# Performance work log

Measured on AMD Instinct MI355X. Metric: run time of the kernel, lower is better.

The kernel has to match this reference:

```python
import jax, jax.numpy as jnp
import numpy as np

WINDOW = 11
SIGMA = 1.5
K1 = 0.01
K2 = 0.03
L = 1.0


def _gauss_kernel(dtype):
    coords = jnp.arange(WINDOW, dtype=dtype) - (WINDOW - 1) / 2.0
    g = jnp.exp(-coords ** 2 / (2.0 * SIGMA ** 2))
    g = g / g.sum()
    return jnp.outer(g, g)  # [k, k]


def setup_inputs() -> dict:
    key = jax.random.key(0)
    k1, k2 = jax.random.split(key)
    B, T, H, W = 8, 16, 256, 256
    return {
        "predicted": jax.random.normal(k1, (B, T, H, W, 1), dtype=jnp.float32),
        "target": jax.random.normal(k2, (B, T, H, W, 1), dtype=jnp.float32),
    }


def reference(predicted, target):
    B, T, H, W, C = predicted.shape
    dt = predicted.dtype
    eps = jnp.asarray(1e-6, dt)

    # valid mask: samples whose target sums to zero are excluded (weighted mean)
    valid = (jnp.sum(target, axis=(1, 2, 3, 4)) != 0).astype(dt)  # [B]

    # per-sample, per-channel min-max normalization over (T, H, W)
    def norm(x):
        mn = jnp.min(x, axis=(1, 2, 3), keepdims=True)
        mx = jnp.max(x, axis=(1, 2, 3), keepdims=True)
        return (x - mn) / jnp.maximum(mx - mn, eps)

    p = norm(predicted)
    t = norm(target)

    # batch all (B,T) single-channel images through one conv: NCHW with N = B*T
    img1 = t.reshape(B * T, 1, H, W)  # original uses target as img1
    img2 = p.reshape(B * T, 1, H, W)
    kern = _gauss_kernel(dt).reshape(1, 1, WINDOW, WINDOW)
    pad = WINDOW // 2

    def conv(x):
        return jax.lax.conv_general_dilated(x, kern, (1, 1), [(pad, pad), (pad, pad)])

    mu1 = conv(img1)
    mu2 = conv(img2)
    mu1_sq = mu1 * mu1
    mu2_sq = mu2 * mu2
    mu1_mu2 = mu1 * mu2
    sigma1_sq = jnp.maximum(conv(img1 * img1) - mu1_sq, eps)
    sigma2_sq = jnp.maximum(conv(img2 * img2) - mu2_sq, eps)
    sigma12 = conv(img1 * img2) - mu1_mu2

    C1 = (K1 * L) ** 2
    C2 = (K2 * L) ** 2
    C3 = C2 / 2.0
    root = jnp.sqrt(sigma1_sq * sigma2_sq)
    luminance = (2.0 * mu1_mu2 + C1) / (mu1_sq + mu2_sq + C1)
    contrast = (2.0 * root + C2) / (sigma1_sq + sigma2_sq + C2)
    structure = (sigma12 + C3) / (root + C3)
    ssim_map = luminance * contrast * structure  # [B*T, 1, H, W]

    # per-(b,t) pixel mean, then mean over T == mean over (T,H,W)
    ssim_per_sample = ssim_map.reshape(B, T, H, W).mean(axis=(1, 2, 3))  # [B]

    n_valid = jnp.maximum(jnp.sum(valid), jnp.asarray(1.0, dt))
    loss = jnp.sum((1.0 - ssim_per_sample) * valid) / n_valid
    return loss
```

## Files before the change

kernel.cpp:

```cpp
#include <hip/hip_runtime.h>
#include <math.h>

#define BB 8
#define TT 16
#define HH 256
#define WW 256
#define NPX (TT * HH * WW)
#define CROWS 32
#define NBLK (BB * TT * (HH / CROWS))

#define P_MINP 0
#define P_MAXP 512
#define P_MINT 1024
#define P_MAXT 1536
#define P_SUMT 2048
#define WS_S   2560

typedef float v2f __attribute__((ext_vector_type(2)));

#define G0 0.0010283776f
#define G1 0.0075987582f
#define G2 0.0360008014f
#define G3 0.1093606427f
#define G4 0.2130055745f
#define G5 0.2660117857f
#define GA_(k) ((k) == 0 || (k) == 10 ? G0 : (k) == 1 || (k) == 9 ? G1 \
              : (k) == 2 || (k) == 8 ? G2 : (k) == 3 || (k) == 7 ? G3 \
              : (k) == 4 || (k) == 6 ? G4 : G5)

__global__ __launch_bounds__(256) void k_reduce(const float* __restrict__ p,
                                                const float* __restrict__ t,
                                                float* __restrict__ wsf) {
  const int b = blockIdx.x >> 6;
  const size_t base = (size_t)b * NPX + (size_t)(blockIdx.x & 63) * (NPX / 64);
  const int tid = threadIdx.x;

  float mnp = 3.4e38f, mxp = -3.4e38f, mnt = 3.4e38f, mxt = -3.4e38f, st = 0.f;
  const float4* p4 = (const float4*)(p + base);
  const float4* t4 = (const float4*)(t + base);
#pragma unroll 4
  for (int it = 0; it < 16; ++it) {
    float4 a = p4[it * 256 + tid];
    float4 c = t4[it * 256 + tid];
    mnp = fminf(mnp, fminf(fminf(a.x, a.y), fminf(a.z, a.w)));
    mxp = fmaxf(mxp, fmaxf(fmaxf(a.x, a.y), fmaxf(a.z, a.w)));
    mnt = fminf(mnt, fminf(fminf(c.x, c.y), fminf(c.z, c.w)));
    mxt = fmaxf(mxt, fmaxf(fmaxf(c.x, c.y), fmaxf(c.z, c.w)));
    st += c.x + c.y + c.z + c.w;
  }
  for (int off = 32; off > 0; off >>= 1) {
    mnp = fminf(mnp, __shfl_down(mnp, off));
    mxp = fmaxf(mxp, __shfl_down(mxp, off));
    mnt = fminf(mnt, __shfl_down(mnt, off));
    mxt = fmaxf(mxt, __shfl_down(mxt, off));
    st += __shfl_down(st, off);
  }
  __shared__ float s_mnp[4], s_mxp[4], s_mnt[4], s_mxt[4], s_st[4];
  int wave = tid >> 6, lane = tid & 63;
  if (lane == 0) {
    s_mnp[wave] = mnp; s_mxp[wave] = mxp;
    s_mnt[wave] = mnt; s_mxt[wave] = mxt; s_st[wave] = st;
  }
  __syncthreads();
  if (tid == 0) {
    for (int w = 1; w < 4; ++w) {
      mnp = fminf(mnp, s_mnp[w]); mxp = fmaxf(mxp, s_mxp[w]);
      mnt = fminf(mnt, s_mnt[w]); mxt = fmaxf(mxt, s_mxt[w]);
      st += s_st[w];
    }
    wsf[P_MINP + blockIdx.x] = mnp;
    wsf[P_MAXP + blockIdx.x] = mxp;
    wsf[P_MINT + blockIdx.x] = mnt;
    wsf[P_MAXT + blockIdx.x] = mxt;
    wsf[P_SUMT + blockIdx.x] = st;
    if (blockIdx.x == 0) wsf[WS_S] = 0.f;
  }
}

#define STEP(J) do {                                                         \
    constexpr int jj = (J);                                                  \
    constexpr int buf = jj & 1;                                              \
    constexpr int slot = jj % 11;                                            \
    const bool in = (unsigned)(ystart + jj) < (unsigned)HH;                  \
    v2f nv;                                                                  \
    nv.x = in ? fmaf(tcur, ts, tb) : 0.f;                                    \
    nv.y = in ? fmaf(pcur, ps, pb) : 0.f;                                    \
    srow[buf][x + 5] = nv;                                                   \
    if constexpr (jj < 41) {                                                 \
      const int yn = min(max(ystart + jj + 1, 0), HH - 1);                   \
      tnxt = tptr[(size_t)yn * WW + x];                                      \
      pnxt = pptr[(size_t)yn * WW + x];                                      \
    }                                                                        \
    __syncthreads();                                                         \
    v2f hmu = {0.f, 0.f}, hsq = {0.f, 0.f};                                  \
    float htp = 0.f;                                                         \
    _Pragma("unroll")                                                        \
    for (int k = 0; k < 11; ++k) {                                           \
      v2f v = srow[buf][x + k];                                              \
      v2f g2 = {GA_(k), GA_(k)};                                             \
      v2f w = g2 * v;                                                        \
      hmu = hmu + w;                                                         \
      hsq = __builtin_elementwise_fma(w, v, hsq);                            \
      htp = fmaf(w.x, v.y, htp);                                             \
    }                                                                        \
    r_mu[slot] = hmu; r_sq[slot] = hsq; r_tp[slot] = htp;                    \
    if constexpr (jj >= 10) {                                                \
      v2f vmu = {0.f, 0.f}, vsq = {0.f, 0.f};                                \
      float vtp = 0.f;                                                       \
      _Pragma("unroll")                                                      \
      for (int k = 0; k < 11; ++k) {                                         \
        const int s = (jj + 1 + k) % 11;                                     \
        v2f g2 = {GA_(k), GA_(k)};                                           \
        vmu = __builtin_elementwise_fma(g2, r_mu[s], vmu);                   \
        vsq = __builtin_elementwise_fma(g2, r_sq[s], vsq);                   \
        vtp = fmaf(GA_(k), r_tp[s], vtp);                                    \
      }                                                                      \
      float m1 = vmu.x, m2 = vmu.y;                                          \
      float mu11 = m1 * m1, mu22 = m2 * m2, m12 = m1 * m2;                   \
      float s1 = fmaxf(vsq.x - mu11, 1e-6f);                                 \
      float s2 = fmaxf(vsq.y - mu22, 1e-6f);                                 \
      float s12 = vtp - m12;                                                 \
      float root = sqrtf(s1 * s2);                                           \
      float num = fmaf(2.f, m12, C1) * fmaf(2.f, root, C2) * (s12 + C3);     \
      float den = (mu11 + mu22 + C1) * (s1 + s2 + C2) * (root + C3);         \
      acc = fmaf(num, __builtin_amdgcn_rcpf(den), acc);                      \
    }                                                                        \
    tcur = tnxt; pcur = pnxt;                                                \
    __builtin_amdgcn_sched_barrier(0);                                       \
  } while (0)

__global__ __launch_bounds__(256, 3) void k_ssim(const float* __restrict__ pred,
                                                 const float* __restrict__ targ,
                                                 float* __restrict__ wsf) {
  const int img = blockIdx.x >> 3;
  const int chunk = blockIdx.x & 7;
  const int b = img >> 4;
  const int x = threadIdx.x;
  const int y0 = chunk * CROWS;
  const float* tptr = targ + (size_t)img * (HH * WW);
  const float* pptr = pred + (size_t)img * (HH * WW);

  __shared__ float sprm[5];
  if (x < 64) {
    float mnp = wsf[P_MINP + b * 64 + x];
    float mxp = wsf[P_MAXP + b * 64 + x];
    float mnt = wsf[P_MINT + b * 64 + x];
    float mxt = wsf[P_MAXT + b * 64 + x];
    float st  = wsf[P_SUMT + b * 64 + x];
    for (int off = 32; off > 0; off >>= 1) {
      mnp = fminf(mnp, __shfl_down(mnp, off));
      mxp = fmaxf(mxp, __shfl_down(mxp, off));
      mnt = fminf(mnt, __shfl_down(mnt, off));
      mxt = fmaxf(mxt, __shfl_down(mxt, off));
      st += __shfl_down(st, off);
    }
    if (x == 0) {
      float psv = 1.f / fmaxf(mxp - mnp, 1e-6f);
      float tsv = 1.f / fmaxf(mxt - mnt, 1e-6f);
      sprm[0] = psv; sprm[1] = -mnp * psv;
      sprm[2] = tsv; sprm[3] = -mnt * tsv;
      sprm[4] = (st != 0.f) ? 1.f : 0.f;
    }
  }

  __shared__ v2f srow[2][WW + 12];
  if (x < 5) {
    v2f z = {0.f, 0.f};
    srow[0][x] = z; srow[1][x] = z;
    srow[0][WW + 5 + x] = z; srow[1][WW + 5 + x] = z;
  }
  __syncthreads();
  const float ps = sprm[0], pb = sprm[1], ts = sprm[2], tb = sprm[3];

  v2f r_mu[11], r_sq[11];
  float r_tp[11];
  float acc = 0.f;
  const int ystart = y0 - 5;
  const float C1 = 1e-4f, C2 = 9e-4f, C3 = 4.5e-4f;

  float tcur, pcur, tnxt = 0.f, pnxt = 0.f;
  {
    const int yc = min(max(ystart, 0), HH - 1);
    tcur = tptr[(size_t)yc * WW + x];
    pcur = pptr[(size_t)yc * WW + x];
  }

  STEP(0);  STEP(1);  STEP(2);  STEP(3);  STEP(4);  STEP(5);  STEP(6);
  STEP(7);  STEP(8);  STEP(9);  STEP(10); STEP(11); STEP(12); STEP(13);
  STEP(14); STEP(15); STEP(16); STEP(17); STEP(18); STEP(19); STEP(20);
  STEP(21); STEP(22); STEP(23); STEP(24); STEP(25); STEP(26); STEP(27);
  STEP(28); STEP(29); STEP(30); STEP(31); STEP(32); STEP(33); STEP(34);
  STEP(35); STEP(36); STEP(37); STEP(38); STEP(39); STEP(40); STEP(41);

  for (int off = 32; off > 0; off >>= 1) acc += __shfl_down(acc, off);
  __shared__ float sred[4];
  if ((x & 63) == 0) sred[x >> 6] = acc;
  __syncthreads();
  if (x == 0) {
    float v = sred[0] + sred[1] + sred[2] + sred[3];
    atomicAdd(&wsf[WS_S], v * sprm[4]);
  }
}

__global__ void k_loss(const float* __restrict__ wsf, float* __restrict__ out) {
  const int c = threadIdx.x;
  float sums[8];
#pragma unroll
  for (int b = 0; b < 8; ++b) sums[b] = wsf[P_SUMT + b * 64 + c];
  for (int off = 32; off > 0; off >>= 1) {
#pragma unroll
    for (int b = 0; b < 8; ++b) sums[b] += __shfl_down(sums[b], off);
  }
  if (c == 0) {
    float sv = 0.f;
#pragma unroll
    for (int b = 0; b < 8; ++b) sv += (sums[b] != 0.f) ? 1.f : 0.f;
    float S = wsf[WS_S];
    out[0] = (sv - S * (1.f / (float)NPX)) / fmaxf(sv, 1.f);
  }
}

extern "C" void kernel_launch(void* const* d_in, const int* in_sizes, int n_in,
                              void* d_out, int out_size, void* d_ws, size_t ws_size,
                              hipStream_t stream) {
  const float* pred = (const float*)d_in[0];
  const float* targ = (const float*)d_in[1];
  float* wsf = (float*)d_ws;
  float* out = (float*)d_out;

  hipLaunchKernelGGL(k_reduce, dim3(512), dim3(256), 0, stream, pred, targ, wsf);
  hipLaunchKernelGGL(k_ssim, dim3(NBLK), dim3(256), 0, stream, pred, targ, wsf);
  hipLaunchKernelGGL(k_loss, dim3(1), dim3(64), 0, stream, wsf, out);
}
```

Before: 132.5 us.

## Halve SSIM row chunk, raise occupancy, fold loss kernel into last block

Cuts rows per block from 32 to 16, doubling the grid and raising the launch-bounds occupancy target from 3 to 6 blocks per CU. The final loss computation moves into the last-finishing SSIM block through an atomic counter, which removes one kernel launch. The sched_barrier mask is loosened so the compiler can move some instructions across steps. In exchange, the 10-row halo is now recomputed over 26 steps for 16 output rows instead of 42 steps for 32, so redundant vertical work rises sharply, and register pressure is capped tighter.

```diff
diff --git a/kernel.cpp b/kernel.cpp
--- a/kernel.cpp
+++ b/kernel.cpp
@@ -6,7 +6,8 @@
 #define HH 256
 #define WW 256
 #define NPX (TT * HH * WW)
-#define CROWS 32
+#define CROWS 16
+#define NSTEP (CROWS + 10)
 #define NBLK (BB * TT * (HH / CROWS))
 
 #define P_MINP 0
@@ -15,6 +16,7 @@
 #define P_MAXT 1536
 #define P_SUMT 2048
 #define WS_S   2560
+#define WS_CNT 2561
 
 typedef float v2f __attribute__((ext_vector_type(2)));
 
@@ -73,7 +75,10 @@
     wsf[P_MINT + blockIdx.x] = mnt;
     wsf[P_MAXT + blockIdx.x] = mxt;
     wsf[P_SUMT + blockIdx.x] = st;
-    if (blockIdx.x == 0) wsf[WS_S] = 0.f;
+    if (blockIdx.x == 0) {
+      wsf[WS_S] = 0.f;
+      ((unsigned*)wsf)[WS_CNT] = 0u;
+    }
   }
 }
 
@@ -86,7 +91,7 @@
     nv.x = in ? fmaf(tcur, ts, tb) : 0.f;                                    \
     nv.y = in ? fmaf(pcur, ps, pb) : 0.f;                                    \
     srow[buf][x + 5] = nv;                                                   \
-    if constexpr (jj < 41) {                                                 \
+    if constexpr (jj < NSTEP - 1) {                                          \
       const int yn = min(max(ystart + jj + 1, 0), HH - 1);                   \
       tnxt = tptr[(size_t)yn * WW + x];                                      \
       pnxt = pptr[(size_t)yn * WW + x];                                      \
@@ -126,14 +131,15 @@
       acc = fmaf(num, __builtin_amdgcn_rcpf(den), acc);                      \
     }                                                                        \
     tcur = tnxt; pcur = pnxt;                                                \
-    __builtin_amdgcn_sched_barrier(0);                                       \
+    __builtin_amdgcn_sched_barrier(0x0007);                                  \
   } while (0)
 
-__global__ __launch_bounds__(256, 3) void k_ssim(const float* __restrict__ pred,
+__global__ __launch_bounds__(256, 6) void k_ssim(const float* __restrict__ pred,
                                                  const float* __restrict__ targ,
-                                                 float* __restrict__ wsf) {
-  const int img = blockIdx.x >> 3;
-  const int chunk = blockIdx.x & 7;
+                                                 float* __restrict__ wsf,
+                                                 float* __restrict__ out) {
+  const int img = blockIdx.x >> 4;
+  const int chunk = blockIdx.x & 15;
   const int b = img >> 4;
   const int x = threadIdx.x;
   const int y0 = chunk * CROWS;
@@ -188,35 +194,39 @@
   STEP(0);  STEP(1);  STEP(2);  STEP(3);  STEP(4);  STEP(5);  STEP(6);
   STEP(7);  STEP(8);  STEP(9);  STEP(10); STEP(11); STEP(12); STEP(13);
   STEP(14); STEP(15); STEP(16); STEP(17); STEP(18); STEP(19); STEP(20);
-  STEP(21); STEP(22); STEP(23); STEP(24); STEP(25); STEP(26); STEP(27);
-  STEP(28); STEP(29); STEP(30); STEP(31); STEP(32); STEP(33); STEP(34);
-  STEP(35); STEP(36); STEP(37); STEP(38); STEP(39); STEP(40); STEP(41);
+  STEP(21); STEP(22); STEP(23); STEP(24); STEP(25);
 
   for (int off = 32; off > 0; off >>= 1) acc += __shfl_down(acc, off);
   __shared__ float sred[4];
+  __shared__ bool sdone;
   if ((x & 63) == 0) sred[x >> 6] = acc;
   __syncthreads();
   if (x == 0) {
     float v = sred[0] + sred[1] + sred[2] + sred[3];
     atomicAdd(&wsf[WS_S], v * sprm[4]);
-  }
-}
-
-__global__ void k_loss(const float* __restrict__ wsf, float* __restrict__ out) {
-  const int c = threadIdx.x;
-  float sums[8];
+    __threadfence();
+    unsigned n = atomicAdd(&((unsigned*)wsf)[WS_CNT], 1u);
+    sdone = (n == NBLK - 1);
+  }
+  __syncthreads();
+  if (sdone) {
+    __threadfence();
+    float sums[8];
+    if (x < 64) {
 #pragma unroll
-  for (int b = 0; b < 8; ++b) sums[b] = wsf[P_SUMT + b * 64 + c];
-  for (int off = 32; off > 0; off >>= 1) {
+      for (int sb = 0; sb < 8; ++sb) sums[sb] = wsf[P_SUMT + sb * 64 + x];
+      for (int off = 32; off > 0; off >>= 1) {
 #pragma unroll
-    for (int b = 0; b < 8; ++b) sums[b] += __shfl_down(sums[b], off);
-  }
-  if (c == 0) {
-    float sv = 0.f;
+        for (int sb = 0; sb < 8; ++sb) sums[sb] += __shfl_down(sums[sb], off);
+      }
+    }
+    if (x == 0) {
+      float sv = 0.f;
 #pragma unroll
-    for (int b = 0; b < 8; ++b) sv += (sums[b] != 0.f) ? 1.f : 0.f;
-    float S = wsf[WS_S];
-    out[0] = (sv - S * (1.f / (float)NPX)) / fmaxf(sv, 1.f);
+      for (int sb = 0; sb < 8; ++sb) sv += (sums[sb] != 0.f) ? 1.f : 0.f;
+      float S = atomicAdd(&wsf[WS_S], 0.f);
+      out[0] = (sv - S * (1.f / (float)NPX)) / fmaxf(sv, 1.f);
+    }
   }
 }
 
@@ -229,6 +239,5 @@
   float* out = (float*)d_out;
 
   hipLaunchKernelGGL(k_reduce, dim3(512), dim3(256), 0, stream, pred, targ, wsf);
-  hipLaunchKernelGGL(k_ssim, dim3(NBLK), dim3(256), 0, stream, pred, targ, wsf);
-  hipLaunchKernelGGL(k_loss, dim3(1), dim3(64), 0, stream, wsf, out);
+  hipLaunchKernelGGL(k_ssim, dim3(NBLK), dim3(256), 0, stream, pred, targ, wsf, out);
 }
```

After: 237.6 us. 79.4% more time.

## Batch four rows per barrier with 8-slot LDS ring and deeper prefetch

Applied to the files above, without the earlier changes.

Restructures the per-row loop so each phase prefetches four input rows into registers, computes four rows from shared memory, then writes the next four normalized rows and syncs once. This cuts block barriers from one per row to one per four rows, and raises the global-load prefetch distance to hide latency. In exchange it needs an 8-slot shared-memory ring instead of double buffering, plus extra prefetch registers, which may reduce occupancy under the 3-blocks launch bound.

```diff
diff --git a/kernel.cpp b/kernel.cpp
--- a/kernel.cpp
+++ b/kernel.cpp
@@ -7,6 +7,8 @@
 #define WW 256
 #define NPX (TT * HH * WW)
 #define CROWS 32
+#define NROWS (CROWS + 10)
+#define NSLOT 8
 #define NBLK (BB * TT * (HH / CROWS))
 
 #define P_MINP 0
@@ -77,56 +79,64 @@
   }
 }
 
-#define STEP(J) do {                                                         \
-    constexpr int jj = (J);                                                  \
-    constexpr int buf = jj & 1;                                              \
-    constexpr int slot = jj % 11;                                            \
-    const bool in = (unsigned)(ystart + jj) < (unsigned)HH;                  \
-    v2f nv;                                                                  \
-    nv.x = in ? fmaf(tcur, ts, tb) : 0.f;                                    \
-    nv.y = in ? fmaf(pcur, ps, pb) : 0.f;                                    \
-    srow[buf][x + 5] = nv;                                                   \
-    if constexpr (jj < 41) {                                                 \
-      const int yn = min(max(ystart + jj + 1, 0), HH - 1);                   \
-      tnxt = tptr[(size_t)yn * WW + x];                                      \
-      pnxt = pptr[(size_t)yn * WW + x];                                      \
-    }                                                                        \
-    __syncthreads();                                                         \
-    v2f hmu = {0.f, 0.f}, hsq = {0.f, 0.f};                                  \
-    float htp = 0.f;                                                         \
-    _Pragma("unroll")                                                        \
-    for (int k = 0; k < 11; ++k) {                                           \
-      v2f v = srow[buf][x + k];                                              \
-      v2f g2 = {GA_(k), GA_(k)};                                             \
-      v2f w = g2 * v;                                                        \
-      hmu = hmu + w;                                                         \
-      hsq = __builtin_elementwise_fma(w, v, hsq);                            \
-      htp = fmaf(w.x, v.y, htp);                                             \
-    }                                                                        \
-    r_mu[slot] = hmu; r_sq[slot] = hsq; r_tp[slot] = htp;                    \
-    if constexpr (jj >= 10) {                                                \
-      v2f vmu = {0.f, 0.f}, vsq = {0.f, 0.f};                                \
-      float vtp = 0.f;                                                       \
-      _Pragma("unroll")                                                      \
-      for (int k = 0; k < 11; ++k) {                                         \
-        const int s = (jj + 1 + k) % 11;                                     \
-        v2f g2 = {GA_(k), GA_(k)};                                           \
-        vmu = __builtin_elementwise_fma(g2, r_mu[s], vmu);                   \
-        vsq = __builtin_elementwise_fma(g2, r_sq[s], vsq);                   \
-        vtp = fmaf(GA_(k), r_tp[s], vtp);                                    \
-      }                                                                      \
-      float m1 = vmu.x, m2 = vmu.y;                                          \
-      float mu11 = m1 * m1, mu22 = m2 * m2, m12 = m1 * m2;                   \
-      float s1 = fmaxf(vsq.x - mu11, 1e-6f);                                 \
-      float s2 = fmaxf(vsq.y - mu22, 1e-6f);                                 \
-      float s12 = vtp - m12;                                                 \
-      float root = sqrtf(s1 * s2);                                           \
-      float num = fmaf(2.f, m12, C1) * fmaf(2.f, root, C2) * (s12 + C3);     \
-      float den = (mu11 + mu22 + C1) * (s1 + s2 + C2) * (root + C3);         \
-      acc = fmaf(num, __builtin_amdgcn_rcpf(den), acc);                      \
-    }                                                                        \
-    tcur = tnxt; pcur = pnxt;                                                \
-    __builtin_amdgcn_sched_barrier(0);                                       \
+
+#define LOADR(R) do { constexpr int r_ = (R); if constexpr (r_ < NROWS) {     \
+    const int yc_ = min(max(ystart + r_, 0), HH - 1);                          \
+    tpre[r_ & 3] = tptr[(size_t)yc_ * WW + x];                                 \
+    ppre[r_ & 3] = pptr[(size_t)yc_ * WW + x];                                 \
+  } } while (0)
+
+#define WRITER(R) do { constexpr int r_ = (R); if constexpr (r_ < NROWS) {     \
+    const bool in_ = (unsigned)(ystart + r_) < (unsigned)HH;                   \
+    v2f nv_;                                                                   \
+    nv_.x = in_ ? fmaf(tpre[r_ & 3], ts, tb) : 0.f;                            \
+    nv_.y = in_ ? fmaf(ppre[r_ & 3], ps, pb) : 0.f;                            \
+    srow[r_ & (NSLOT - 1)][x + 5] = nv_;                                       \
+  } } while (0)
+
+#define CSTEP(R) do { constexpr int r_ = (R); if constexpr (r_ < NROWS) {      \
+    constexpr int slot_ = r_ % 11;                                             \
+    v2f hmu = {0.f, 0.f}, hsq = {0.f, 0.f};                                    \
+    float htp = 0.f;                                                           \
+    _Pragma("unroll")                                                          \
+    for (int k = 0; k < 11; ++k) {                                             \
+      v2f v = srow[r_ & (NSLOT - 1)][x + k];                                   \
+      v2f g2 = {GA_(k), GA_(k)};                                               \
+      v2f w = g2 * v;                                                          \
+      hmu = hmu + w;                                                           \
+      hsq = __builtin_elementwise_fma(w, v, hsq);                              \
+      htp = fmaf(w.x, v.y, htp);                                               \
+    }                                                                          \
+    r_mu[slot_] = hmu; r_sq[slot_] = hsq; r_tp[slot_] = htp;                   \
+    if constexpr (r_ >= 10) {                                                  \
+      v2f vmu = {0.f, 0.f}, vsq = {0.f, 0.f};                                  \
+      float vtp = 0.f;                                                         \
+      _Pragma("unroll")                                                        \
+      for (int k = 0; k < 11; ++k) {                                           \
+        const int s = (r_ + 1 + k) % 11;                                       \
+        v2f g2 = {GA_(k), GA_(k)};                                             \
+        vmu = __builtin_elementwise_fma(g2, r_mu[s], vmu);                     \
+        vsq = __builtin_elementwise_fma(g2, r_sq[s], vsq);                     \
+        vtp = fmaf(GA_(k), r_tp[s], vtp);                                      \
+      }                                                                        \
+      float m1 = vmu.x, m2 = vmu.y;                                            \
+      float mu11 = m1 * m1, mu22 = m2 * m2, m12 = m1 * m2;                     \
+      float s1 = fmaxf(vsq.x - mu11, 1e-6f);                                   \
+      float s2 = fmaxf(vsq.y - mu22, 1e-6f);                                   \
+      float s12 = vtp - m12;                                                   \
+      float root = sqrtf(s1 * s2);                                             \
+      float num = fmaf(2.f, m12, C1) * fmaf(2.f, root, C2) * (s12 + C3);       \
+      float den = (mu11 + mu22 + C1) * (s1 + s2 + C2) * (root + C3);           \
+      acc = fmaf(num, __builtin_amdgcn_rcpf(den), acc);                        \
+    }                                                                          \
+  } } while (0)
+
+#define PHASE(P) do {                                                          \
+    LOADR(4*(P)+4); LOADR(4*(P)+5); LOADR(4*(P)+6); LOADR(4*(P)+7);            \
+    CSTEP(4*(P)+0); CSTEP(4*(P)+1); CSTEP(4*(P)+2); CSTEP(4*(P)+3);            \
+    WRITER(4*(P)+4); WRITER(4*(P)+5); WRITER(4*(P)+6); WRITER(4*(P)+7);        \
+    __syncthreads();                                                           \
+    __builtin_amdgcn_sched_barrier(0);                                         \
   } while (0)
 
 __global__ __launch_bounds__(256, 3) void k_ssim(const float* __restrict__ pred,
@@ -163,11 +173,14 @@
     }
   }
 
-  __shared__ v2f srow[2][WW + 12];
+  __shared__ v2f srow[NSLOT][WW + 12];
   if (x < 5) {
     v2f z = {0.f, 0.f};
-    srow[0][x] = z; srow[1][x] = z;
-    srow[0][WW + 5 + x] = z; srow[1][WW + 5 + x] = z;
+#pragma unroll
+    for (int s = 0; s < NSLOT; ++s) {
+      srow[s][x] = z;
+      srow[s][WW + 5 + x] = z;
+    }
   }
   __syncthreads();
   const float ps = sprm[0], pb = sprm[1], ts = sprm[2], tb = sprm[3];
@@ -178,19 +191,16 @@
   const int ystart = y0 - 5;
   const float C1 = 1e-4f, C2 = 9e-4f, C3 = 4.5e-4f;
 
-  float tcur, pcur, tnxt = 0.f, pnxt = 0.f;
-  {
-    const int yc = min(max(ystart, 0), HH - 1);
-    tcur = tptr[(size_t)yc * WW + x];
-    pcur = pptr[(size_t)yc * WW + x];
-  }
-
-  STEP(0);  STEP(1);  STEP(2);  STEP(3);  STEP(4);  STEP(5);  STEP(6);
-  STEP(7);  STEP(8);  STEP(9);  STEP(10); STEP(11); STEP(12); STEP(13);
-  STEP(14); STEP(15); STEP(16); STEP(17); STEP(18); STEP(19); STEP(20);
-  STEP(21); STEP(22); STEP(23); STEP(24); STEP(25); STEP(26); STEP(27);
-  STEP(28); STEP(29); STEP(30); STEP(31); STEP(32); STEP(33); STEP(34);
-  STEP(35); STEP(36); STEP(37); STEP(38); STEP(39); STEP(40); STEP(41);
+  float tpre[4], ppre[4];
+
+  LOADR(0); LOADR(1); LOADR(2); LOADR(3);
+  WRITER(0); WRITER(1); WRITER(2); WRITER(3);
+  __syncthreads();
+  __builtin_amdgcn_sched_barrier(0);
+
+  PHASE(0); PHASE(1); PHASE(2); PHASE(3); PHASE(4);
+  PHASE(5); PHASE(6); PHASE(7); PHASE(8); PHASE(9);
+  CSTEP(40); CSTEP(41);
 
   for (int off = 32; off > 0; off >>= 1) acc += __shfl_down(acc, off);
   __shared__ float sred[4];
```

Result: no change. 134.1 us (+1.2%).
